# Performance work log

Hardware: AMD Instinct MI355X
Metric: run time of the kernel (lower is better)

## Reference

```python
import jax, jax.numpy as jnp
import numpy as np

N = 4096  # number of image features; must equal D because forward does attn @ img_feats.T
D = 4096


def setup_inputs() -> dict:
    key = jax.random.key(0)
    img_feats = jax.random.normal(key, (N, D), dtype=jnp.float32)
    return {"img_feats": img_feats}


def reference(img_feats):
    d = img_feats.shape[-1]
    x = img_feats / jnp.sqrt(jnp.asarray(d, img_feats.dtype))
    sims = x @ x.T  # [N, N] self-similarity
    n = sims.shape[0]
    idx = jnp.arange(n)
    sims = sims.at[idx, idx].set(-jnp.inf)  # mask self-similarity on the diagonal
    attn = jax.nn.softmax(sims, axis=-1)  # [N, N]
    return attn @ x.T  # [N, N] (requires N == D, as in the original)
```

## Files before the change

kernel.cpp:

```cpp
#include <hip/hip_runtime.h>
#include <hip/hip_bf16.h>
#include <stdint.h>

#define N 4096
#define BM 128
#define SK 128
#define PM 256
#define PN 256
#define PK 64

typedef __hip_bfloat16 bf16;
typedef __attribute__((ext_vector_type(8))) __bf16 bfrag;
typedef __attribute__((ext_vector_type(4))) float floatx4;
typedef __attribute__((ext_vector_type(8))) int i32x8;
typedef __attribute__((ext_vector_type(4))) int i32x4;

__device__ __forceinline__ void gld_lds16(const void* g, void* l) {
    __builtin_amdgcn_global_load_lds(
        (const __attribute__((address_space(1))) void*)g,
        (__attribute__((address_space(3))) void*)l, 16, 0, 0);
}

__device__ __forceinline__ unsigned short f2bf(float x) {
    __hip_bfloat16 h = __float2bfloat16(x);
    return *(unsigned short*)&h;
}

#define PV_BAR()   __builtin_amdgcn_s_barrier()
#define PV_LGKM0() asm volatile("s_waitcnt lgkmcnt(0)" ::: "memory")
#define PV_VM4()   asm volatile("s_waitcnt vmcnt(4)" ::: "memory")

__global__ __launch_bounds__(256) void cvt_scale(const float* __restrict__ in,
                                                 unsigned short* __restrict__ xb,
                                                 uint8_t* __restrict__ x8,
                                                 float* __restrict__ rowsum) {
    if (blockIdx.x < 16) rowsum[blockIdx.x * 256 + threadIdx.x] = 0.f;
    const long i = ((long)blockIdx.x * 256 + threadIdx.x) * 8;
    float4 a = *(const float4*)(in + i);
    float4 b = *(const float4*)(in + i + 4);
    const float sc = 0.015625f;
    float v[8] = {a.x, a.y, a.z, a.w, b.x, b.y, b.z, b.w};
    alignas(16) unsigned short r[8];
#pragma unroll
    for (int k = 0; k < 8; ++k) r[k] = f2bf(v[k] * sc);
    *(uint4*)(xb + i) = *(const uint4*)r;

    int p0 = __builtin_amdgcn_cvt_pk_fp8_f32(v[0], v[1], 0, false);
    p0     = __builtin_amdgcn_cvt_pk_fp8_f32(v[2], v[3], p0, true);
    int p1 = __builtin_amdgcn_cvt_pk_fp8_f32(v[4], v[5], 0, false);
    p1     = __builtin_amdgcn_cvt_pk_fp8_f32(v[6], v[7], p1, true);
    int2 pk; pk.x = p0; pk.y = p1;
    *(int2*)(x8 + i) = pk;
}

__global__ __launch_bounds__(256) void gemm_sym(const uint8_t* __restrict__ X8,
                                                unsigned short* __restrict__ E,
                                                float* __restrict__ rowsum) {
    __shared__ __align__(16) uint8_t smem[65536];

    const int t    = threadIdx.x;
    const int lane = t & 63;
    const int wave = t >> 6;
    const int wm   = wave >> 1;
    const int wn   = wave & 1;
    const int l15  = lane & 15;
    const int l7   = lane & 7;
    const int q    = lane >> 4;

    const int b0 = blockIdx.x;
    const int b  = (b0 & 7) * 66 + (b0 >> 3);
    int I = (int)((sqrtf((float)(8 * b + 1)) - 1.0f) * 0.5f);
    if ((I + 1) * (I + 2) / 2 <= b) ++I;
    if (I * (I + 1) / 2 > b) --I;
    const int Jb = b - I * (I + 1) / 2;
    const int bm = I * BM;
    const int bn = Jb * BM;
    const bool diag = (I == Jb);

    floatx4 acc[4][4] = {};

    const int srow = t >> 3;
    const int x_   = (t & 7) ^ (srow & 7);
    const int skb  = ((x_ & 3) << 1) | (x_ >> 2);
    const uint8_t* Ag = X8 + (long)(bm + srow) * N + skb * 16;
    const uint8_t* Bg = X8 + (long)(bn + srow) * N + skb * 16;

#pragma unroll
    for (int i = 0; i < 4; ++i) {
        gld_lds16(Ag + (long)i * 32 * N, smem + t * 16 + i * 4096);
        gld_lds16(Bg + (long)i * 32 * N, smem + 16384 + t * 16 + i * 4096);
    }
    __syncthreads();

    int cur = 0;
    for (int k0 = 0; k0 < N; k0 += SK) {
        if (k0 + SK < N) {
            uint8_t* An = smem + (cur ^ 1) * 32768 + t * 16;
#pragma unroll
            for (int i = 0; i < 4; ++i) {
                gld_lds16(Ag + (long)i * 32 * N + k0 + SK, An + i * 4096);
                gld_lds16(Bg + (long)i * 32 * N + k0 + SK, An + 16384 + i * 4096);
            }
        }

        const uint8_t* As = smem + cur * 32768;
        const uint8_t* Bs = As + 16384;
        i32x8 af[4], bfr[4];
#pragma unroll
        for (int i = 0; i < 4; ++i) {
            const int row = wm * 64 + i * 16 + l15;
            i32x4 lo = *(const i32x4*)&As[(row * 8 + (q ^ l7)) * 16];
            i32x4 hi = *(const i32x4*)&As[(row * 8 + ((4 + q) ^ l7)) * 16];
            af[i] = (i32x8){lo.x, lo.y, lo.z, lo.w, hi.x, hi.y, hi.z, hi.w};
        }
#pragma unroll
        for (int j = 0; j < 4; ++j) {
            const int row = wn * 64 + j * 16 + l15;
            i32x4 lo = *(const i32x4*)&Bs[(row * 8 + (q ^ l7)) * 16];
            i32x4 hi = *(const i32x4*)&Bs[(row * 8 + ((4 + q) ^ l7)) * 16];
            bfr[j] = (i32x8){lo.x, lo.y, lo.z, lo.w, hi.x, hi.y, hi.z, hi.w};
        }
#pragma unroll
        for (int i = 0; i < 4; ++i)
#pragma unroll
            for (int j = 0; j < 4; ++j)
                acc[i][j] = __builtin_amdgcn_mfma_scale_f32_16x16x128_f8f6f4(
                    af[i], bfr[j], acc[i][j],
                    0, 0,
                    0, 0x79797979,
                    0, 0x79797979);
        __syncthreads();
        cur ^= 1;
    }

    const int col0 = bn + wn * 64 + l15;
    const int row0 = bm + wm * 64 + q * 4;

#pragma unroll
    for (int i = 0; i < 4; ++i) {
#pragma unroll
        for (int r = 0; r < 4; ++r) {
            const int row = row0 + i * 16 + r;
            float rs = 0.f;
#pragma unroll
            for (int j = 0; j < 4; ++j) {
                const int col = col0 + j * 16;
                float e = (row == col) ? 0.f : __expf(acc[i][j][r]);
                acc[i][j][r] = e;
                rs += e;
                E[(long)row * N + col] = f2bf(e);
            }
#pragma unroll
            for (int off = 1; off < 16; off <<= 1) rs += __shfl_xor(rs, off);
            if (l15 == 0) atomicAdd(rowsum + row, rs);
        }
    }

    if (!diag) {
#pragma unroll
        for (int j = 0; j < 4; ++j) {
            float cs = 0.f;
#pragma unroll
            for (int i = 0; i < 4; ++i)
#pragma unroll
                for (int r = 0; r < 4; ++r) cs += acc[i][j][r];
            cs += __shfl_xor(cs, 16);
            cs += __shfl_xor(cs, 32);
            if (q == 0) atomicAdd(rowsum + bn + wn * 64 + j * 16 + l15, cs);
        }

        unsigned short* tb = (unsigned short*)smem + wave * 4096;
        __syncthreads();
#pragma unroll
        for (int i = 0; i < 4; ++i) {
            const int lr0 = i * 16 + q * 4;
            const int blk = lr0 >> 3;
            const int half = (lr0 >> 2) & 1;
#pragma unroll
            for (int j = 0; j < 4; ++j) {
                const int lc = j * 16 + l15;
                union { unsigned short u[4]; uint2 v2; } pk;
#pragma unroll
                for (int r = 0; r < 4; ++r) pk.u[r] = f2bf(acc[i][j][r]);
                *(uint2*)&tb[lc * 64 + 8 * (blk ^ (lc & 7)) + 4 * half] = pk.v2;
            }
        }
        __syncthreads();

        const int gr0 = lane >> 3;
        const int cb  = lane & 7;
#pragma unroll
        for (int p = 0; p < 8; ++p) {
            const int gr = p * 8 + gr0;
            uint4 v = *(const uint4*)&tb[gr * 64 + 8 * (cb ^ (gr & 7))];
            *(uint4*)&E[(long)(bn + wn * 64 + gr) * N + bm + wm * 64 + cb * 8] = v;
        }
    }
}

#define PV_STAGE_A(buf, h, k0) do { \
    const bf16* s_ = Asrc + (h) * 128 * (long)N + (k0); \
    bf16* d_ = dstl + (buf) * 16384 + (h) * 8192; \
    gld_lds16(s_, d_); \
    gld_lds16(s_ + 64 * (long)N, d_ + 4096); } while (0)

#define PV_STAGE_B(buf, h, k0) do { \
    const bf16* s_ = Bsrc + (h) * 128 * (long)N + (k0); \
    bf16* d_ = dstl + 32768 + (buf) * 16384 + (h) * 8192; \
    gld_lds16(s_, d_); \
    gld_lds16(s_ + 64 * (long)N, d_ + 4096); } while (0)

#define PV_LDA(buf, mi) do { \
    const bf16* b_ = lds + (buf) * 16384; \
    _Pragma("unroll") for (int f_ = 0; f_ < 4; ++f_) { \
      const int r_ = wm * 128 + (mi) * 64 + f_ * 16 + l15; \
      ar[f_][0] = *(const bfrag*)&b_[(r_ * 8 + (q ^ l7)) * 8]; \
      ar[f_][1] = *(const bfrag*)&b_[(r_ * 8 + ((4 + q) ^ l7)) * 8]; } } while (0)

#define PV_LDB(buf, nj) do { \
    const bf16* b_ = lds + 32768 + (buf) * 16384; \
    _Pragma("unroll") for (int g_ = 0; g_ < 2; ++g_) { \
      const int r_ = wn * 64 + (nj) * 32 + g_ * 16 + l15; \
      br[nj][g_][0] = *(const bfrag*)&b_[(r_ * 8 + (q ^ l7)) * 8]; \
      br[nj][g_][1] = *(const bfrag*)&b_[(r_ * 8 + ((4 + q) ^ l7)) * 8]; } } while (0)

#define PV_MM(mi, nj) do { \
    __builtin_amdgcn_s_setprio(1); \
    _Pragma("unroll") for (int f_ = 0; f_ < 4; ++f_) \
    _Pragma("unroll") for (int g_ = 0; g_ < 2; ++g_) \
    _Pragma("unroll") for (int k_ = 0; k_ < 2; ++k_) \
      acc[(mi)*4+f_][(nj)*2+g_] = __builtin_amdgcn_mfma_f32_16x16x32_bf16( \
          ar[f_][k_], br[nj][g_][k_], acc[(mi)*4+f_][(nj)*2+g_], 0, 0, 0); \
    __builtin_amdgcn_s_setprio(0); } while (0)

__global__ __launch_bounds__(512, 2) void gemm_pv(const bf16* __restrict__ A,
                                                  const bf16* __restrict__ B,
                                                  float* __restrict__ C,
                                                  const float* __restrict__ rowsum) {
    __shared__ __align__(16) bf16 lds[4 * 16384];

    const int t    = threadIdx.x;
    const int lane = t & 63;
    const int wm   = (t >> 6) >> 2;
    const int wn   = (t >> 6) & 3;
    const int l15  = lane & 15;
    const int l7   = lane & 7;
    const int q    = lane >> 4;

    const int swz = (blockIdx.x & 7) * 32 + (blockIdx.x >> 3);
    const int bm  = (swz >> 4) * PM;
    const int bn  = (swz & 15) * PN;

    const int srow = t >> 3;
    const int skb  = (t & 7) ^ (srow & 7);
    const bf16* Asrc = A + (long)(bm + srow) * N + skb * 8;
    const bf16* Bsrc = B + (long)(bn + srow) * N + skb * 8;
    bf16* dstl = lds + t * 8;

    floatx4 acc[8][4] = {};
    bfrag ar[4][2], br[2][2][2];

    PV_STAGE_B(0, 0, 0); PV_STAGE_B(0, 1, 0);
    PV_STAGE_A(0, 0, 0); PV_STAGE_A(0, 1, 0);
    PV_STAGE_B(1, 0, PK); PV_STAGE_B(1, 1, PK);
    PV_VM4();
    PV_BAR();

    for (int i = 0; i < 32; ++i) {
        const int ka1 = ((2 * i + 1) * PK) & (N - 1);
        const int kb2 = ((2 * i + 2) * PK) & (N - 1);
        const int kb3 = ((2 * i + 3) * PK) & (N - 1);
        PV_LDA(0, 0); PV_LDB(0, 0); PV_STAGE_A(1, 0, ka1);
        PV_BAR(); PV_LGKM0();
        PV_MM(0, 0);
        PV_BAR();
        PV_LDB(0, 1); PV_STAGE_A(1, 1, ka1);
        PV_BAR(); PV_LGKM0();
        PV_MM(0, 1);
        PV_BAR();
        PV_LDA(0, 1); PV_STAGE_B(0, 0, kb2);
        PV_BAR(); PV_LGKM0();
        PV_MM(1, 1);
        PV_BAR();
        PV_STAGE_B(0, 1, kb2);
        PV_BAR();
        PV_MM(1, 0);
        PV_VM4(); PV_BAR();
        PV_LDA(1, 0); PV_LDB(1, 0); PV_STAGE_A(0, 0, kb2);
        PV_BAR(); PV_LGKM0();
        PV_MM(0, 0);
        PV_BAR();
        PV_LDB(1, 1); PV_STAGE_A(0, 1, kb2);
        PV_BAR(); PV_LGKM0();
        PV_MM(0, 1);
        PV_BAR();
        PV_LDA(1, 1); PV_STAGE_B(1, 0, kb3);
        PV_BAR(); PV_LGKM0();
        PV_MM(1, 1);
        PV_BAR();
        PV_STAGE_B(1, 1, kb3);
        PV_BAR();
        PV_MM(1, 0);
        PV_VM4(); PV_BAR();
    }

    const int rowbase = bm + wm * 128 + q * 4;
    const int colbase = bn + wn * 64 + l15;
#pragma unroll
    for (int f = 0; f < 8; ++f) {
#pragma unroll
        for (int r = 0; r < 4; ++r) {
            const int row = rowbase + f * 16 + r;
            const float inv = 1.0f / rowsum[row];
#pragma unroll
            for (int g = 0; g < 4; ++g)
                C[(long)row * N + colbase + g * 16] = acc[f][g][r] * inv;
        }
    }
}

extern "C" void kernel_launch(void* const* d_in, const int* in_sizes, int n_in,
                              void* d_out, int out_size, void* d_ws, size_t ws_size,
                              hipStream_t stream) {
    const float* in = (const float*)d_in[0];
    float* out = (float*)d_out;

    float* rowsum = (float*)d_ws;
    bf16* xb = (bf16*)((char*)d_ws + 16384);
    unsigned short* E = (unsigned short*)((char*)d_ws + 16384 + (size_t)N * N * sizeof(bf16));
    uint8_t* x8 = (uint8_t*)d_out;

    cvt_scale<<<(N * (long)N) / (256 * 8), 256, 0, stream>>>(
        in, (unsigned short*)xb, x8, rowsum);

    gemm_sym<<<528, 256, 0, stream>>>(x8, E, rowsum);
    gemm_pv<<<256, 512, 0, stream>>>((const bf16*)E, xb, out, rowsum);
}
```

Baseline: 275.0 us.

## Run PV GEMM in FP8 with offset-shifted exp encoding and column-sum correction

Switches the second GEMM (attn @ x^T) from bf16 to fp8 MFMA with block scales. The unnormalized exp values are stored as 16*(e-1) in fp8 to keep precision, and a per-row sum of x (sv, computed in the convert kernel) corrects the offset in the epilogue. The separate bf16 copy of x is dropped and the rowsum zeroing becomes a memset. This halves the bytes loaded for the PV GEMM and doubles MFMA throughput, at the cost of lower-precision probabilities and an LDS footprint that doubles to 128KB per block, which may limit occupancy or fail to fit.

```diff
diff --git a/kernel.cpp b/kernel.cpp
--- a/kernel.cpp
+++ b/kernel.cpp
@@ -7,10 +7,8 @@
 #define SK 128
 #define PM 256
 #define PN 256
-#define PK 64
-
-typedef __hip_bfloat16 bf16;
-typedef __attribute__((ext_vector_type(8))) __bf16 bfrag;
+#define PK8 128
+
 typedef __attribute__((ext_vector_type(4))) float floatx4;
 typedef __attribute__((ext_vector_type(8))) int i32x8;
 typedef __attribute__((ext_vector_type(4))) int i32x4;
@@ -21,9 +19,8 @@
         (__attribute__((address_space(3))) void*)l, 16, 0, 0);
 }
 
-__device__ __forceinline__ unsigned short f2bf(float x) {
-    __hip_bfloat16 h = __float2bfloat16(x);
-    return *(unsigned short*)&h;
+__device__ __forceinline__ uint8_t f2fp8(float x) {
+    return (uint8_t)(__builtin_amdgcn_cvt_pk_fp8_f32(x, x, 0, false) & 0xFF);
 }
 
 #define PV_BAR()   __builtin_amdgcn_s_barrier()
@@ -31,19 +28,12 @@
 #define PV_VM4()   asm volatile("s_waitcnt vmcnt(4)" ::: "memory")
 
 __global__ __launch_bounds__(256) void cvt_scale(const float* __restrict__ in,
-                                                 unsigned short* __restrict__ xb,
                                                  uint8_t* __restrict__ x8,
-                                                 float* __restrict__ rowsum) {
-    if (blockIdx.x < 16) rowsum[blockIdx.x * 256 + threadIdx.x] = 0.f;
+                                                 float* __restrict__ sv) {
     const long i = ((long)blockIdx.x * 256 + threadIdx.x) * 8;
     float4 a = *(const float4*)(in + i);
     float4 b = *(const float4*)(in + i + 4);
-    const float sc = 0.015625f;
     float v[8] = {a.x, a.y, a.z, a.w, b.x, b.y, b.z, b.w};
-    alignas(16) unsigned short r[8];
-#pragma unroll
-    for (int k = 0; k < 8; ++k) r[k] = f2bf(v[k] * sc);
-    *(uint4*)(xb + i) = *(const uint4*)r;
 
     int p0 = __builtin_amdgcn_cvt_pk_fp8_f32(v[0], v[1], 0, false);
     p0     = __builtin_amdgcn_cvt_pk_fp8_f32(v[2], v[3], p0, true);
@@ -51,10 +41,15 @@
     p1     = __builtin_amdgcn_cvt_pk_fp8_f32(v[6], v[7], p1, true);
     int2 pk; pk.x = p0; pk.y = p1;
     *(int2*)(x8 + i) = pk;
+
+    float partial = (v[0] + v[1] + v[2] + v[3] + v[4] + v[5] + v[6] + v[7]) * 0.015625f;
+#pragma unroll
+    for (int off = 1; off < 64; off <<= 1) partial += __shfl_xor(partial, off);
+    if ((threadIdx.x & 63) == 0) atomicAdd(sv + (int)(i >> 12), partial);
 }
 
 __global__ __launch_bounds__(256) void gemm_sym(const uint8_t* __restrict__ X8,
-                                                unsigned short* __restrict__ E,
+                                                uint8_t* __restrict__ F8,
                                                 float* __restrict__ rowsum) {
     __shared__ __align__(16) uint8_t smem[65536];
 
@@ -146,9 +141,10 @@
             for (int j = 0; j < 4; ++j) {
                 const int col = col0 + j * 16;
                 float e = (row == col) ? 0.f : __expf(acc[i][j][r]);
-                acc[i][j][r] = e;
                 rs += e;
-                E[(long)row * N + col] = f2bf(e);
+                float f = 16.0f * (e - 1.0f);
+                acc[i][j][r] = f;
+                F8[(long)row * N + col] = f2fp8(f);
             }
 #pragma unroll
             for (int off = 1; off < 16; off <<= 1) rs += __shfl_xor(rs, off);
@@ -159,85 +155,86 @@
     if (!diag) {
 #pragma unroll
         for (int j = 0; j < 4; ++j) {
-            float cs = 0.f;
+            float csf = 0.f;
 #pragma unroll
             for (int i = 0; i < 4; ++i)
 #pragma unroll
-                for (int r = 0; r < 4; ++r) cs += acc[i][j][r];
+                for (int r = 0; r < 4; ++r) csf += acc[i][j][r];
+            float cs = 16.0f + csf * 0.0625f;
             cs += __shfl_xor(cs, 16);
             cs += __shfl_xor(cs, 32);
             if (q == 0) atomicAdd(rowsum + bn + wn * 64 + j * 16 + l15, cs);
         }
 
-        unsigned short* tb = (unsigned short*)smem + wave * 4096;
+        uint8_t* tb = smem + wave * 4096;
         __syncthreads();
 #pragma unroll
         for (int i = 0; i < 4; ++i) {
-            const int lr0 = i * 16 + q * 4;
-            const int blk = lr0 >> 3;
-            const int half = (lr0 >> 2) & 1;
+            const int g = i * 4 + q;
 #pragma unroll
             for (int j = 0; j < 4; ++j) {
                 const int lc = j * 16 + l15;
-                union { unsigned short u[4]; uint2 v2; } pk;
-#pragma unroll
-                for (int r = 0; r < 4; ++r) pk.u[r] = f2bf(acc[i][j][r]);
-                *(uint2*)&tb[lc * 64 + 8 * (blk ^ (lc & 7)) + 4 * half] = pk.v2;
+                int w = __builtin_amdgcn_cvt_pk_fp8_f32(acc[i][j][0], acc[i][j][1], 0, false);
+                w     = __builtin_amdgcn_cvt_pk_fp8_f32(acc[i][j][2], acc[i][j][3], w, true);
+                *(int*)&tb[lc * 64 + 4 * (g ^ (l15 & 12))] = w;
             }
         }
         __syncthreads();
 
-        const int gr0 = lane >> 3;
-        const int cb  = lane & 7;
-#pragma unroll
-        for (int p = 0; p < 8; ++p) {
-            const int gr = p * 8 + gr0;
-            uint4 v = *(const uint4*)&tb[gr * 64 + 8 * (cb ^ (gr & 7))];
-            *(uint4*)&E[(long)(bn + wn * 64 + gr) * N + bm + wm * 64 + cb * 8] = v;
+        const int gr = lane;
+        const long ebase = (long)(bn + wn * 64 + gr) * N + bm + wm * 64;
+#pragma unroll
+        for (int c = 0; c < 4; ++c) {
+            uint4 v = *(const uint4*)&tb[gr * 64 + 16 * (c ^ ((gr >> 2) & 3))];
+            *(uint4*)&F8[ebase + 16 * c] = v;
         }
     }
 }
 
 #define PV_STAGE_A(buf, h, k0) do { \
-    const bf16* s_ = Asrc + (h) * 128 * (long)N + (k0); \
-    bf16* d_ = dstl + (buf) * 16384 + (h) * 8192; \
+    const uint8_t* s_ = Asrc + (h) * 128 * (long)N + (k0); \
+    uint8_t* d_ = dstl + (buf) * 32768 + (h) * 16384; \
     gld_lds16(s_, d_); \
-    gld_lds16(s_ + 64 * (long)N, d_ + 4096); } while (0)
+    gld_lds16(s_ + 64 * (long)N, d_ + 8192); } while (0)
 
 #define PV_STAGE_B(buf, h, k0) do { \
-    const bf16* s_ = Bsrc + (h) * 128 * (long)N + (k0); \
-    bf16* d_ = dstl + 32768 + (buf) * 16384 + (h) * 8192; \
+    const uint8_t* s_ = Bsrc + (h) * 128 * (long)N + (k0); \
+    uint8_t* d_ = dstl + 65536 + (buf) * 32768 + (h) * 16384; \
     gld_lds16(s_, d_); \
-    gld_lds16(s_ + 64 * (long)N, d_ + 4096); } while (0)
+    gld_lds16(s_ + 64 * (long)N, d_ + 8192); } while (0)
 
 #define PV_LDA(buf, mi) do { \
-    const bf16* b_ = lds + (buf) * 16384; \
+    const uint8_t* b_ = lds8 + (buf) * 32768; \
     _Pragma("unroll") for (int f_ = 0; f_ < 4; ++f_) { \
       const int r_ = wm * 128 + (mi) * 64 + f_ * 16 + l15; \
-      ar[f_][0] = *(const bfrag*)&b_[(r_ * 8 + (q ^ l7)) * 8]; \
-      ar[f_][1] = *(const bfrag*)&b_[(r_ * 8 + ((4 + q) ^ l7)) * 8]; } } while (0)
+      i32x4 lo_ = *(const i32x4*)&b_[(r_ * 8 + (q ^ l7)) * 16]; \
+      i32x4 hi_ = *(const i32x4*)&b_[(r_ * 8 + ((4 + q) ^ l7)) * 16]; \
+      ar[f_] = (i32x8){lo_.x, lo_.y, lo_.z, lo_.w, hi_.x, hi_.y, hi_.z, hi_.w}; } } while (0)
 
 #define PV_LDB(buf, nj) do { \
-    const bf16* b_ = lds + 32768 + (buf) * 16384; \
+    const uint8_t* b_ = lds8 + 65536 + (buf) * 32768; \
     _Pragma("unroll") for (int g_ = 0; g_ < 2; ++g_) { \
       const int r_ = wn * 64 + (nj) * 32 + g_ * 16 + l15; \
-      br[nj][g_][0] = *(const bfrag*)&b_[(r_ * 8 + (q ^ l7)) * 8]; \
-      br[nj][g_][1] = *(const bfrag*)&b_[(r_ * 8 + ((4 + q) ^ l7)) * 8]; } } while (0)
+      i32x4 lo_ = *(const i32x4*)&b_[(r_ * 8 + (q ^ l7)) * 16]; \
+      i32x4 hi_ = *(const i32x4*)&b_[(r_ * 8 + ((4 + q) ^ l7)) * 16]; \
+      br[nj][g_] = (i32x8){lo_.x, lo_.y, lo_.z, lo_.w, hi_.x, hi_.y, hi_.z, hi_.w}; } } while (0)
 
 #define PV_MM(mi, nj) do { \
     __builtin_amdgcn_s_setprio(1); \
     _Pragma("unroll") for (int f_ = 0; f_ < 4; ++f_) \
     _Pragma("unroll") for (int g_ = 0; g_ < 2; ++g_) \
-    _Pragma("unroll") for (int k_ = 0; k_ < 2; ++k_) \
-      acc[(mi)*4+f_][(nj)*2+g_] = __builtin_amdgcn_mfma_f32_16x16x32_bf16( \
-          ar[f_][k_], br[nj][g_][k_], acc[(mi)*4+f_][(nj)*2+g_], 0, 0, 0); \
+      acc[(mi)*4+f_][(nj)*2+g_] = __builtin_amdgcn_mfma_scale_f32_16x16x128_f8f6f4( \
+          ar[f_], br[nj][g_], acc[(mi)*4+f_][(nj)*2+g_], \
+          0, 0, 0, 0x7B7B7B7B,       \
+          0, 0x79797979);            \
     __builtin_amdgcn_s_setprio(0); } while (0)
 
-__global__ __launch_bounds__(512, 2) void gemm_pv(const bf16* __restrict__ A,
-                                                  const bf16* __restrict__ B,
+__global__ __launch_bounds__(512, 2) void gemm_pv(const uint8_t* __restrict__ A,
+                                                  const uint8_t* __restrict__ B,
                                                   float* __restrict__ C,
-                                                  const float* __restrict__ rowsum) {
-    __shared__ __align__(16) bf16 lds[4 * 16384];
+                                                  const float* __restrict__ rowsum,
+                                                  const float* __restrict__ sv) {
+    __shared__ __align__(16) uint8_t lds8[131072];
 
     const int t    = threadIdx.x;
     const int lane = t & 63;
@@ -252,24 +249,25 @@
     const int bn  = (swz & 15) * PN;
 
     const int srow = t >> 3;
-    const int skb  = (t & 7) ^ (srow & 7);
-    const bf16* Asrc = A + (long)(bm + srow) * N + skb * 8;
-    const bf16* Bsrc = B + (long)(bn + srow) * N + skb * 8;
-    bf16* dstl = lds + t * 8;
+    const int x_   = (t & 7) ^ (srow & 7);
+    const int skb  = ((x_ & 3) << 1) | (x_ >> 2);
+    const uint8_t* Asrc = A + (long)(bm + srow) * N + skb * 16;
+    const uint8_t* Bsrc = B + (long)(bn + srow) * N + skb * 16;
+    uint8_t* dstl = lds8 + t * 16;
 
     floatx4 acc[8][4] = {};
-    bfrag ar[4][2], br[2][2][2];
+    i32x8 ar[4], br[2][2];
 
     PV_STAGE_B(0, 0, 0); PV_STAGE_B(0, 1, 0);
     PV_STAGE_A(0, 0, 0); PV_STAGE_A(0, 1, 0);
-    PV_STAGE_B(1, 0, PK); PV_STAGE_B(1, 1, PK);
+    PV_STAGE_B(1, 0, PK8); PV_STAGE_B(1, 1, PK8);
     PV_VM4();
     PV_BAR();
 
-    for (int i = 0; i < 32; ++i) {
-        const int ka1 = ((2 * i + 1) * PK) & (N - 1);
-        const int kb2 = ((2 * i + 2) * PK) & (N - 1);
-        const int kb3 = ((2 * i + 3) * PK) & (N - 1);
+    for (int i = 0; i < 16; ++i) {
+        const int ka1 = ((2 * i + 1) * PK8) & (N - 1);
+        const int kb2 = ((2 * i + 2) * PK8) & (N - 1);
+        const int kb3 = ((2 * i + 3) * PK8) & (N - 1);
         PV_LDA(0, 0); PV_LDB(0, 0); PV_STAGE_A(1, 0, ka1);
         PV_BAR(); PV_LGKM0();
         PV_MM(0, 0);
@@ -306,6 +304,9 @@
 
     const int rowbase = bm + wm * 128 + q * 4;
     const int colbase = bn + wn * 64 + l15;
+    float sj[4];
+#pragma unroll
+    for (int g = 0; g < 4; ++g) sj[g] = sv[colbase + g * 16];
 #pragma unroll
     for (int f = 0; f < 8; ++f) {
 #pragma unroll
@@ -314,7 +315,7 @@
             const float inv = 1.0f / rowsum[row];
 #pragma unroll
             for (int g = 0; g < 4; ++g)
-                C[(long)row * N + colbase + g * 16] = acc[f][g][r] * inv;
+                C[(long)row * N + colbase + g * 16] = (acc[f][g][r] + sj[g]) * inv;
         }
     }
 }
@@ -326,13 +327,14 @@
     float* out = (float*)d_out;
 
     float* rowsum = (float*)d_ws;
-    bf16* xb = (bf16*)((char*)d_ws + 16384);
-    unsigned short* E = (unsigned short*)((char*)d_ws + 16384 + (size_t)N * N * sizeof(bf16));
-    uint8_t* x8 = (uint8_t*)d_out;
-
-    cvt_scale<<<(N * (long)N) / (256 * 8), 256, 0, stream>>>(
-        in, (unsigned short*)xb, x8, rowsum);
-
-    gemm_sym<<<528, 256, 0, stream>>>(x8, E, rowsum);
-    gemm_pv<<<256, 512, 0, stream>>>((const bf16*)E, xb, out, rowsum);
-}
+    float* sv     = (float*)((char*)d_ws + 16384);
+    uint8_t* x8   = (uint8_t*)d_ws + 32768;
+    uint8_t* F8   = x8 + (size_t)N * N;
+
+    hipMemsetAsync(d_ws, 0, 32768, stream);
+
+    cvt_scale<<<(N * (long)N) / (256 * 8), 256, 0, stream>>>(in, x8, sv);
+
+    gemm_sym<<<528, 256, 0, stream>>>(x8, F8, rowsum);
+    gemm_pv<<<256, 512, 0, stream>>>(F8, x8, out, rowsum, sv);
+}
```

New measurement: 359.6 us. 30.8% more time.
